# Optimization experiments

Hardware: AMD Instinct MI355X
Metric: run time of the kernel (lower is better)

## Reference

```python
import jax, jax.numpy as jnp
import numpy as np

# Sampled-neighborhood sizes (NeighborSampler-style shrinking hops)
N0, N1, N2, N3 = 200000, 50000, 12500, 3200
E0, E1, E2 = 500000, 125000, 32000
D_IN, D_H, D_OUT = 128, 256, 128


def setup_inputs() -> dict:
    key = jax.random.key(0)
    ks = jax.random.split(key, 16)
    x = jax.random.normal(ks[0], (N0, D_IN), dtype=jnp.float32)
    src0 = jax.random.randint(ks[1], (E0,), 0, N0)
    dst0 = jax.random.randint(ks[2], (E0,), 0, N1)
    src1 = jax.random.randint(ks[3], (E1,), 0, N1)
    dst1 = jax.random.randint(ks[4], (E1,), 0, N2)
    src2 = jax.random.randint(ks[5], (E2,), 0, N2)
    dst2 = jax.random.randint(ks[6], (E2,), 0, N3)
    s = 0.05
    # SAGEConv params: lin_l (applied to aggregated neighbors, has bias), lin_r (root)
    wl0 = jax.random.normal(ks[7], (D_H, D_IN), dtype=jnp.float32) * s
    wr0 = jax.random.normal(ks[8], (D_H, D_IN), dtype=jnp.float32) * s
    b0 = jnp.zeros((D_H,), dtype=jnp.float32)
    wl1 = jax.random.normal(ks[9], (D_H, D_H), dtype=jnp.float32) * s
    wr1 = jax.random.normal(ks[10], (D_H, D_H), dtype=jnp.float32) * s
    b1 = jnp.zeros((D_H,), dtype=jnp.float32)
    wl2 = jax.random.normal(ks[11], (D_OUT, D_H), dtype=jnp.float32) * s
    wr2 = jax.random.normal(ks[12], (D_OUT, D_H), dtype=jnp.float32) * s
    b2 = jnp.zeros((D_OUT,), dtype=jnp.float32)
    return {"x": x, "src0": src0, "dst0": dst0, "src1": src1, "dst1": dst1,
            "src2": src2, "dst2": dst2,
            "wl0": wl0, "wr0": wr0, "b0": b0,
            "wl1": wl1, "wr1": wr1, "b1": b1,
            "wl2": wl2, "wr2": wr2, "b2": b2}


def _sage(x, src, dst, n_tgt, wl, wr, b):
    """Bipartite SAGEConv with mean aggregation (PyG default)."""
    x_tgt = x[:n_tgt]                                   # [n_tgt, d_in]
    msg = x[src]                                        # [E, d_in] gather
    s = jax.ops.segment_sum(msg, dst, num_segments=n_tgt)
    cnt = jax.ops.segment_sum(jnp.ones((src.shape[0], 1), x.dtype), dst,
                              num_segments=n_tgt)
    mean = s / jnp.maximum(cnt, 1.0)                    # mean over in-neighbors
    return mean @ wl.T + b + x_tgt @ wr.T               # [n_tgt, d_out]


def reference(x, src0, dst0, src1, dst1, src2, dst2,
              wl0, wr0, b0, wl1, wr1, b1, wl2, wr2, b2):
    h = jax.nn.relu(_sage(x, src0, dst0, N1, wl0, wr0, b0))
    h = jax.nn.relu(_sage(h, src1, dst1, N2, wl1, wr1, b1))
    return _sage(h, src2, dst2, N3, wl2, wr2, b2)       # [N3, D_OUT]
```

## Files before the change

kernel.cpp:

```cpp
#include <hip/hip_runtime.h>

#define N0s 200000
#define N1s 50000
#define N2s 12500
#define N3s 3200
#define E0s 500000
#define E1s 125000
#define E2s 32000
#define D_INs 128
#define D_Hs 256
#define D_OUTs 128

#define CAP 64
#define LOGCAP 6

#define GSTRIDE 72
#define CSTRIDE 132

#define XN4 (N0s * D_INs / 4)
#define WN4 65536
#define CAST_TOTAL (XN4 + WN4)
#define CAST_BLOCKS ((CAST_TOTAL + 2047) / 2048)

typedef __attribute__((ext_vector_type(8))) short short8;
typedef __attribute__((ext_vector_type(4))) float floatx4;

__device__ __forceinline__ unsigned short f32_to_bf16_rne(float f) {
    unsigned int u = __float_as_uint(f);
    u += 0x7fffu + ((u >> 16) & 1u);
    return (unsigned short)(u >> 16);
}
__device__ __forceinline__ float bf16_to_f32(unsigned short h) {
    return __uint_as_float(((unsigned int)h) << 16);
}

struct CastArgs {
    const float* x; unsigned short* xb;
    const float* ws_[6]; unsigned short* wd[6];
};

__launch_bounds__(256)
__global__ void cast_all(CastArgs a)
{
    #pragma unroll
    for (int j = 0; j < 8; ++j) {
        int i = blockIdx.x * 2048 + j * 256 + threadIdx.x;
        if (i < XN4) {
            float4 v = *(const float4*)&a.x[(size_t)i * 4];
            ushort4 o;
            o.x = f32_to_bf16_rne(v.x);
            o.y = f32_to_bf16_rne(v.y);
            o.z = f32_to_bf16_rne(v.z);
            o.w = f32_to_bf16_rne(v.w);
            *(ushort4*)&a.xb[(size_t)i * 4] = o;
        } else if (i < CAST_TOTAL) {
            int g = i - XN4;
            int seg, base;
            if      (g < 8192)  { seg = 0; base = 0; }
            else if (g < 16384) { seg = 1; base = 8192; }
            else if (g < 32768) { seg = 2; base = 16384; }
            else if (g < 49152) { seg = 3; base = 32768; }
            else if (g < 57344) { seg = 4; base = 49152; }
            else                { seg = 5; base = 57344; }
            int k = g - base;
            float4 v = *(const float4*)&a.ws_[seg][(size_t)k * 4];
            ushort4 o;
            o.x = f32_to_bf16_rne(v.x);
            o.y = f32_to_bf16_rne(v.y);
            o.z = f32_to_bf16_rne(v.z);
            o.w = f32_to_bf16_rne(v.w);
            *(ushort4*)&a.wd[seg][(size_t)k * 4] = o;
        }
    }
}

struct Bins {
    const int *src0, *dst0, *src1, *dst1, *src2, *dst2;
    int *cnt0, *cnt1, *cnt2;
    int *eidx0, *eidx1, *eidx2;
};

__launch_bounds__(256)
__global__ void fill3(Bins b)
{
    int e = blockIdx.x * 256 + threadIdx.x;
    if (e < E0s) {
        int d = b.dst0[e];
        int p = atomicAdd(&b.cnt0[d], 1);
        if (p < CAP) b.eidx0[(d << LOGCAP) + p] = b.src0[e];
    } else if (e < E0s + E1s) {
        int i = e - E0s;
        int d = b.dst1[i];
        int p = atomicAdd(&b.cnt1[d], 1);
        if (p < CAP) b.eidx1[(d << LOGCAP) + p] = b.src1[i];
    } else if (e < E0s + E1s + E2s) {
        int i = e - E0s - E1s;
        int d = b.dst2[i];
        int p = atomicAdd(&b.cnt2[d], 1);
        if (p < CAP) b.eidx2[(d << LOGCAP) + p] = b.src2[i];
    }
}

__launch_bounds__(256)
__global__ void gather_mean(const unsigned short* __restrict__ X,
                            const int* __restrict__ eidx,
                            const int* __restrict__ cnt,
                            unsigned short* __restrict__ out,
                            int n_tgt, int D, int logTpr)
{
    int gid = blockIdx.x * 256 + threadIdx.x;
    int row = gid >> logTpr;
    if (row >= n_tgt) return;
    int c = (gid & ((1 << logTpr) - 1)) << 2;

    int deg = cnt[row];
    int e = min(deg, CAP);
    const int* bp = &eidx[row << LOGCAP];

    float a0 = 0.f, a1 = 0.f, a2 = 0.f, a3 = 0.f;
    int i = 0;
    for (; i + 2 <= e; i += 2) {
        int s0 = bp[i], s1 = bp[i + 1];
        ushort4 v0 = *(const ushort4*)&X[(size_t)s0 * D + c];
        ushort4 v1 = *(const ushort4*)&X[(size_t)s1 * D + c];
        a0 += bf16_to_f32(v0.x) + bf16_to_f32(v1.x);
        a1 += bf16_to_f32(v0.y) + bf16_to_f32(v1.y);
        a2 += bf16_to_f32(v0.z) + bf16_to_f32(v1.z);
        a3 += bf16_to_f32(v0.w) + bf16_to_f32(v1.w);
    }
    if (i < e) {
        ushort4 v0 = *(const ushort4*)&X[(size_t)bp[i] * D + c];
        a0 += bf16_to_f32(v0.x); a1 += bf16_to_f32(v0.y);
        a2 += bf16_to_f32(v0.z); a3 += bf16_to_f32(v0.w);
    }
    float inv = 1.0f / fmaxf((float)deg, 1.0f);
    ushort4 o;
    o.x = f32_to_bf16_rne(a0 * inv);
    o.y = f32_to_bf16_rne(a1 * inv);
    o.z = f32_to_bf16_rne(a2 * inv);
    o.w = f32_to_bf16_rne(a3 * inv);
    *(ushort4*)&out[(size_t)row * D + c] = o;
}

__launch_bounds__(256)
__global__ void mfma_gemm(const unsigned short* __restrict__ A1,
                          const unsigned short* __restrict__ A2,
                          const unsigned short* __restrict__ W1,
                          const unsigned short* __restrict__ W2,
                          const float* __restrict__ bias,
                          void* __restrict__ Cout,
                          int M, int N, int K1, int K2,
                          int relu, int out_bf16)
{
    __shared__ unsigned short smem[2 * 128 * GSTRIDE];
    unsigned short* As = smem;
    unsigned short* Bs = smem + 128 * GSTRIDE;

    const int tid  = threadIdx.x;
    const int wave = tid >> 6;
    const int lane = tid & 63;
    const int quad = lane >> 4;
    const int lr   = lane & 15;
    const int wm   = wave >> 1;
    const int wn   = wave & 1;
    const int row0 = blockIdx.x * 128;
    const int col0 = blockIdx.y * 128;

    floatx4 acc[4][4] = {};

    for (int seg = 0; seg < 2; ++seg) {
        const unsigned short* Ap = (seg == 0) ? A1 : A2;
        const unsigned short* Wp = (seg == 0) ? W1 : W2;
        const int K = (seg == 0) ? K1 : K2;

        for (int k0 = 0; k0 < K; k0 += 64) {
            #pragma unroll
            for (int it = 0; it < 4; ++it) {
                int sid = tid + it * 256;
                int r = sid >> 3;
                int sc = (sid & 7) << 3;
                int gr = min(row0 + r, M - 1);
                uint4 v = *(const uint4*)&Ap[(size_t)gr * K + k0 + sc];
                *(uint4*)&As[r * GSTRIDE + sc] = v;
            }
            #pragma unroll
            for (int it = 0; it < 4; ++it) {
                int sid = tid + it * 256;
                int r = sid >> 3;
                int sc = (sid & 7) << 3;
                uint4 v = *(const uint4*)&Wp[(size_t)(col0 + r) * K + k0 + sc];
                *(uint4*)&Bs[r * GSTRIDE + sc] = v;
            }
            __syncthreads();

            #pragma unroll
            for (int kh = 0; kh < 2; ++kh) {
                short8 afr[4], bfr[4];
                #pragma unroll
                for (int mt = 0; mt < 4; ++mt)
                    afr[mt] = *(const short8*)&As[(wm * 64 + mt * 16 + lr) * GSTRIDE + kh * 32 + quad * 8];
                #pragma unroll
                for (int nt = 0; nt < 4; ++nt)
                    bfr[nt] = *(const short8*)&Bs[(wn * 64 + nt * 16 + lr) * GSTRIDE + kh * 32 + quad * 8];

                #pragma unroll
                for (int mt = 0; mt < 4; ++mt)
                    #pragma unroll
                    for (int nt = 0; nt < 4; ++nt)
                        acc[mt][nt] = __builtin_amdgcn_mfma_f32_16x16x32_bf16(
                            afr[mt], bfr[nt], acc[mt][nt], 0, 0, 0);
            }
            __syncthreads();
        }
    }

    if (out_bf16) {
        unsigned short* Cs = smem;
        #pragma unroll
        for (int nt = 0; nt < 4; ++nt) {
            int col = wn * 64 + nt * 16 + lr;
            float bv = bias[col0 + col];
            #pragma unroll
            for (int mt = 0; mt < 4; ++mt) {
                #pragma unroll
                for (int reg = 0; reg < 4; ++reg) {
                    int row = wm * 64 + mt * 16 + quad * 4 + reg;
                    float v = acc[mt][nt][reg] + bv;
                    if (relu) v = fmaxf(v, 0.f);
                    Cs[row * CSTRIDE + col] = f32_to_bf16_rne(v);
                }
            }
        }
        __syncthreads();
        int r  = tid >> 1;
        int hf = tid & 1;
        int gr = row0 + r;
        if (gr < M) {
            unsigned short* Crow = (unsigned short*)Cout + (size_t)gr * N + col0 + hf * 64;
            #pragma unroll
            for (int j = 0; j < 8; ++j) {
                uint4 v = *(const uint4*)&Cs[r * CSTRIDE + hf * 64 + j * 8];
                *(uint4*)&Crow[j * 8] = v;
            }
        }
    } else {
        #pragma unroll
        for (int nt = 0; nt < 4; ++nt) {
            int gc = col0 + wn * 64 + nt * 16 + lr;
            float bv = bias[gc];
            #pragma unroll
            for (int mt = 0; mt < 4; ++mt) {
                #pragma unroll
                for (int reg = 0; reg < 4; ++reg) {
                    int gr = row0 + wm * 64 + mt * 16 + quad * 4 + reg;
                    if (gr < M) {
                        float v = acc[mt][nt][reg] + bv;
                        if (relu) v = fmaxf(v, 0.f);
                        ((float*)Cout)[(size_t)gr * N + gc] = v;
                    }
                }
            }
        }
    }
}

extern "C" void kernel_launch(void* const* d_in, const int* in_sizes, int n_in,
                              void* d_out, int out_size, void* d_ws, size_t ws_size,
                              hipStream_t stream)
{
    const float* x   = (const float*)d_in[0];
    const int* src0  = (const int*)d_in[1];
    const int* dst0  = (const int*)d_in[2];
    const int* src1  = (const int*)d_in[3];
    const int* dst1  = (const int*)d_in[4];
    const int* src2  = (const int*)d_in[5];
    const int* dst2  = (const int*)d_in[6];
    const float* wl0 = (const float*)d_in[7];
    const float* wr0 = (const float*)d_in[8];
    const float* b0  = (const float*)d_in[9];
    const float* wl1 = (const float*)d_in[10];
    const float* wr1 = (const float*)d_in[11];
    const float* b1  = (const float*)d_in[12];
    const float* wl2 = (const float*)d_in[13];
    const float* wr2 = (const float*)d_in[14];
    const float* b2  = (const float*)d_in[15];

    unsigned short* ws = (unsigned short*)d_ws;
    unsigned short* xb    = ws;
    unsigned short* h1    = xb + (size_t)N0s * D_INs;
    unsigned short* h2    = h1 + (size_t)N1s * D_Hs;
    unsigned short* meanA = h2 + (size_t)N2s * D_Hs;
    unsigned short* wl0b  = meanA + (size_t)N1s * D_INs;
    unsigned short* wr0b  = wl0b + 32768;
    unsigned short* wl1b  = wr0b + 32768;
    unsigned short* wr1b  = wl1b + 65536;
    unsigned short* wl2b  = wr1b + 65536;
    unsigned short* wr2b  = wl2b + 32768;
    int* ib = (int*)(wr2b + 32768);
    int* cnt0 = ib;
    int* cnt1 = cnt0 + 50048;
    int* cnt2 = cnt1 + 12544;
    int* eidx0 = cnt2 + 3264;
    int* eidx1 = eidx0 + (size_t)N1s * CAP;
    int* eidx2 = eidx1 + (size_t)N2s * CAP;

    Bins b;
    b.src0 = src0; b.dst0 = dst0; b.src1 = src1; b.dst1 = dst1;
    b.src2 = src2; b.dst2 = dst2;
    b.cnt0 = cnt0; b.cnt1 = cnt1; b.cnt2 = cnt2;
    b.eidx0 = eidx0; b.eidx1 = eidx1; b.eidx2 = eidx2;

    hipMemsetAsync(cnt0, 0, (50048 + 12544 + 3264) * sizeof(int), stream);
    const int Etot = E0s + E1s + E2s;
    fill3<<<(Etot + 255) / 256, 256, 0, stream>>>(b);

    CastArgs ca;
    ca.x = x; ca.xb = xb;
    ca.ws_[0] = wl0; ca.ws_[1] = wr0; ca.ws_[2] = wl1;
    ca.ws_[3] = wr1; ca.ws_[4] = wl2; ca.ws_[5] = wr2;
    ca.wd[0] = wl0b; ca.wd[1] = wr0b; ca.wd[2] = wl1b;
    ca.wd[3] = wr1b; ca.wd[4] = wl2b; ca.wd[5] = wr2b;
    cast_all<<<CAST_BLOCKS, 256, 0, stream>>>(ca);

    {
        int th = N1s * 32;
        gather_mean<<<(th + 255) / 256, 256, 0, stream>>>(xb, eidx0, cnt0,
                                                          meanA, N1s, D_INs, 5);
        dim3 g((N1s + 127) / 128, D_Hs / 128);
        mfma_gemm<<<g, 256, 0, stream>>>(meanA, xb, wl0b, wr0b, b0, h1,
                                         N1s, D_Hs, D_INs, D_INs, 1, 1);
    }
    {
        int th = N2s * 64;
        gather_mean<<<(th + 255) / 256, 256, 0, stream>>>(h1, eidx1, cnt1,
                                                          meanA, N2s, D_Hs, 6);
        dim3 g((N2s + 127) / 128, D_Hs / 128);
        mfma_gemm<<<g, 256, 0, stream>>>(meanA, h1, wl1b, wr1b, b1, h2,
                                         N2s, D_Hs, D_Hs, D_Hs, 1, 1);
    }
    {
        int th = N3s * 64;
        gather_mean<<<(th + 255) / 256, 256, 0, stream>>>(h2, eidx2, cnt2,
                                                          meanA, N3s, D_Hs, 6);
        dim3 g((N3s + 127) / 128, D_OUTs / 128);
        mfma_gemm<<<g, 256, 0, stream>>>(meanA, h2, wl2b, wr2b, b2, (float*)d_out,
                                         N3s, D_OUTs, D_Hs, D_Hs, 0, 0);
    }
}
```

Baseline: 345.8 us.

## Prefetch GEMM tiles into registers and batch gather index loads

The GEMM loop now loads the next K-tile of A and W into registers while MFMAs run on the current shared-memory tile, merging the two segments into one tile sequence. The gather-mean kernel reads 16 neighbor indices at once with vector loads and issues up to 16 independent row loads per batch, which raises memory-level parallelism. In exchange both kernels use more registers, which may lower occupancy. The wider index loads also rely on the per-row index buffer being padded to CAP.

```diff
diff --git a/kernel.cpp b/kernel.cpp
--- a/kernel.cpp
+++ b/kernel.cpp
@@ -118,21 +118,25 @@
     const int* bp = &eidx[row << LOGCAP];
 
     float a0 = 0.f, a1 = 0.f, a2 = 0.f, a3 = 0.f;
-    int i = 0;
-    for (; i + 2 <= e; i += 2) {
-        int s0 = bp[i], s1 = bp[i + 1];
-        ushort4 v0 = *(const ushort4*)&X[(size_t)s0 * D + c];
-        ushort4 v1 = *(const ushort4*)&X[(size_t)s1 * D + c];
-        a0 += bf16_to_f32(v0.x) + bf16_to_f32(v1.x);
-        a1 += bf16_to_f32(v0.y) + bf16_to_f32(v1.y);
-        a2 += bf16_to_f32(v0.z) + bf16_to_f32(v1.z);
-        a3 += bf16_to_f32(v0.w) + bf16_to_f32(v1.w);
-    }
-    if (i < e) {
-        ushort4 v0 = *(const ushort4*)&X[(size_t)bp[i] * D + c];
-        a0 += bf16_to_f32(v0.x); a1 += bf16_to_f32(v0.y);
-        a2 += bf16_to_f32(v0.z); a3 += bf16_to_f32(v0.w);
-    }
+
+    for (int base = 0; base < e; base += 16) {
+        int idx[16];
+        #pragma unroll
+        for (int q = 0; q < 4; ++q)
+            *(uint4*)&idx[q * 4] = *(const uint4*)&bp[base + q * 4];
+        int m = min(e - base, 16);
+        #pragma unroll
+        for (int j = 0; j < 16; ++j) {
+            if (j < m) {
+                ushort4 v = *(const ushort4*)&X[(size_t)idx[j] * D + c];
+                a0 += bf16_to_f32(v.x);
+                a1 += bf16_to_f32(v.y);
+                a2 += bf16_to_f32(v.z);
+                a3 += bf16_to_f32(v.w);
+            }
+        }
+    }
+
     float inv = 1.0f / fmaxf((float)deg, 1.0f);
     ushort4 o;
     o.x = f32_to_bf16_rne(a0 * inv);
@@ -140,6 +144,30 @@
     o.z = f32_to_bf16_rne(a2 * inv);
     o.w = f32_to_bf16_rne(a3 * inv);
     *(ushort4*)&out[(size_t)row * D + c] = o;
+}
+
+__device__ __forceinline__ void load_tile(const unsigned short* __restrict__ A1,
+                                          const unsigned short* __restrict__ A2,
+                                          const unsigned short* __restrict__ W1,
+                                          const unsigned short* __restrict__ W2,
+                                          int t, int T1, int K1, int K2,
+                                          int tid, int row0, int col0, int M,
+                                          uint4 (&ra)[4], uint4 (&rb)[4])
+{
+    int seg = (t >= T1);
+    const unsigned short* Ap = seg ? A2 : A1;
+    const unsigned short* Wp = seg ? W2 : W1;
+    int K  = seg ? K2 : K1;
+    int k0 = (seg ? (t - T1) : t) << 6;
+    #pragma unroll
+    for (int it = 0; it < 4; ++it) {
+        int sid = tid + it * 256;
+        int r = sid >> 3;
+        int sc = (sid & 7) << 3;
+        int gr = min(row0 + r, M - 1);
+        ra[it] = *(const uint4*)&Ap[(size_t)gr * K + k0 + sc];
+        rb[it] = *(const uint4*)&Wp[(size_t)(col0 + r) * K + k0 + sc];
+    }
 }
 
 __launch_bounds__(256)
@@ -166,55 +194,50 @@
     const int row0 = blockIdx.x * 128;
     const int col0 = blockIdx.y * 128;
 
+    const int T1 = K1 >> 6;
+    const int T  = T1 + (K2 >> 6);
+
     floatx4 acc[4][4] = {};
-
-    for (int seg = 0; seg < 2; ++seg) {
-        const unsigned short* Ap = (seg == 0) ? A1 : A2;
-        const unsigned short* Wp = (seg == 0) ? W1 : W2;
-        const int K = (seg == 0) ? K1 : K2;
-
-        for (int k0 = 0; k0 < K; k0 += 64) {
-            #pragma unroll
-            for (int it = 0; it < 4; ++it) {
-                int sid = tid + it * 256;
-                int r = sid >> 3;
-                int sc = (sid & 7) << 3;
-                int gr = min(row0 + r, M - 1);
-                uint4 v = *(const uint4*)&Ap[(size_t)gr * K + k0 + sc];
-                *(uint4*)&As[r * GSTRIDE + sc] = v;
-            }
-            #pragma unroll
-            for (int it = 0; it < 4; ++it) {
-                int sid = tid + it * 256;
-                int r = sid >> 3;
-                int sc = (sid & 7) << 3;
-                uint4 v = *(const uint4*)&Wp[(size_t)(col0 + r) * K + k0 + sc];
-                *(uint4*)&Bs[r * GSTRIDE + sc] = v;
-            }
-            __syncthreads();
-
-            #pragma unroll
-            for (int kh = 0; kh < 2; ++kh) {
-                short8 afr[4], bfr[4];
-                #pragma unroll
-                for (int mt = 0; mt < 4; ++mt)
-                    afr[mt] = *(const short8*)&As[(wm * 64 + mt * 16 + lr) * GSTRIDE + kh * 32 + quad * 8];
+    uint4 ra[4], rb[4];
+
+    load_tile(A1, A2, W1, W2, 0, T1, K1, K2, tid, row0, col0, M, ra, rb);
+
+    for (int t = 0; t < T; ++t) {
+        __syncthreads();
+        #pragma unroll
+        for (int it = 0; it < 4; ++it) {
+            int sid = tid + it * 256;
+            int r = sid >> 3;
+            int sc = (sid & 7) << 3;
+            *(uint4*)&As[r * GSTRIDE + sc] = ra[it];
+            *(uint4*)&Bs[r * GSTRIDE + sc] = rb[it];
+        }
+        __syncthreads();
+
+        if (t + 1 < T)
+            load_tile(A1, A2, W1, W2, t + 1, T1, K1, K2, tid, row0, col0, M, ra, rb);
+
+        #pragma unroll
+        for (int kh = 0; kh < 2; ++kh) {
+            short8 afr[4], bfr[4];
+            #pragma unroll
+            for (int mt = 0; mt < 4; ++mt)
+                afr[mt] = *(const short8*)&As[(wm * 64 + mt * 16 + lr) * GSTRIDE + kh * 32 + quad * 8];
+            #pragma unroll
+            for (int nt = 0; nt < 4; ++nt)
+                bfr[nt] = *(const short8*)&Bs[(wn * 64 + nt * 16 + lr) * GSTRIDE + kh * 32 + quad * 8];
+
+            #pragma unroll
+            for (int mt = 0; mt < 4; ++mt)
                 #pragma unroll
                 for (int nt = 0; nt < 4; ++nt)
-                    bfr[nt] = *(const short8*)&Bs[(wn * 64 + nt * 16 + lr) * GSTRIDE + kh * 32 + quad * 8];
-
-                #pragma unroll
-                for (int mt = 0; mt < 4; ++mt)
-                    #pragma unroll
-                    for (int nt = 0; nt < 4; ++nt)
-                        acc[mt][nt] = __builtin_amdgcn_mfma_f32_16x16x32_bf16(
-                            afr[mt], bfr[nt], acc[mt][nt], 0, 0, 0);
-            }
-            __syncthreads();
+                    acc[mt][nt] = __builtin_amdgcn_mfma_f32_16x16x32_bf16(
+                        afr[mt], bfr[nt], acc[mt][nt], 0, 0, 0);
         }
     }
 
     if (out_bf16) {
+        __syncthreads();
         unsigned short* Cs = smem;
         #pragma unroll
         for (int nt = 0; nt < 4; ++nt) {
```

Result: slower. 411.2 us (+18.9%).
